# Performance work log

Measured on AMD Instinct MI355X. Metric: run time of the kernel, lower is better.

Reference implementation:

```python
import jax, jax.numpy as jnp
import numpy as np

N, T, F_IN, H, D_FF, C_OUT = 4096, 60, 64, 128, 256, 1


def _gru_layer(x_tnf, W_ih, W_hh, b_ih, b_hh):
    # torch nn.GRU single layer; x_tnf: [T, N, in]
    def step(h, xt):
        gi = xt @ W_ih.T + b_ih          # [N, 3H]
        gh = h @ W_hh.T + b_hh
        i_r, i_z, i_n = jnp.split(gi, 3, axis=-1)
        h_r, h_z, h_n = jnp.split(gh, 3, axis=-1)
        r = jax.nn.sigmoid(i_r + h_r)
        z = jax.nn.sigmoid(i_z + h_z)
        n = jnp.tanh(i_n + r * h_n)
        h = (1.0 - z) * n + z * h
        return h, h
    h0 = jnp.zeros((x_tnf.shape[1], W_hh.shape[1]), x_tnf.dtype)
    hT, ys = jax.lax.scan(step, h0, x_tnf)
    return hT, ys


def setup_inputs() -> dict:
    key = jax.random.key(0)
    ks = jax.random.split(key, 20)
    s_in = 1.0 / np.sqrt(F_IN)
    s_h = 1.0 / np.sqrt(H)
    inp = {
        'x': jax.random.normal(ks[0], (N, T, F_IN), jnp.float32),
        'W_ih0': jax.random.normal(ks[1], (3 * H, F_IN), jnp.float32) * s_in,
        'W_hh0': jax.random.normal(ks[2], (3 * H, H), jnp.float32) * s_h,
        'b_ih0': jax.random.normal(ks[3], (3 * H,), jnp.float32) * s_h,
        'b_hh0': jax.random.normal(ks[4], (3 * H,), jnp.float32) * s_h,
        'W_ih1': jax.random.normal(ks[5], (3 * H, H), jnp.float32) * s_h,
        'W_hh1': jax.random.normal(ks[6], (3 * H, H), jnp.float32) * s_h,
        'b_ih1': jax.random.normal(ks[7], (3 * H,), jnp.float32) * s_h,
        'b_hh1': jax.random.normal(ks[8], (3 * H,), jnp.float32) * s_h,
        'Wt': jax.random.normal(ks[9], (H, H), jnp.float32) * s_h,
        'bt': jax.random.normal(ks[10], (H,), jnp.float32) * s_h,
        'a': jax.random.normal(ks[11], (2 * H, 1), jnp.float32),
        'Wfc': jax.random.normal(ks[12], (H, H), jnp.float32) * s_h,
        'bfc': jax.random.normal(ks[13], (H,), jnp.float32) * s_h,
        'Wp1': jax.random.normal(ks[14], (D_FF, H), jnp.float32) * s_h,
        'bp1': jax.random.normal(ks[15], (D_FF,), jnp.float32) * s_h,
        'Wp2': jax.random.normal(ks[16], (C_OUT, D_FF), jnp.float32) * (1.0 / np.sqrt(D_FF)),
        'bp2': jax.random.normal(ks[17], (C_OUT,), jnp.float32) * (1.0 / np.sqrt(D_FF)),
    }
    return inp


def reference(x, W_ih0, W_hh0, b_ih0, b_hh0, W_ih1, W_hh1, b_ih1, b_hh1,
              Wt, bt, a, Wfc, bfc, Wp1, bp1, Wp2, bp2):
    x_tnf = jnp.transpose(x, (1, 0, 2))  # [T, N, F]
    _, ys0 = _gru_layer(x_tnf, W_ih0, W_hh0, b_ih0, b_hh0)
    hT, _ = _gru_layer(ys0, W_ih1, W_hh1, b_ih1, b_hh1)
    hidden = hT  # out[:, -1, :], [N, H]

    # cal_attention: score[i,j] = a[:H].x_j + a[H:].x_i  (separable GAT score)
    xt = hidden @ Wt.T + bt                      # transformation(x) == transformation(y)
    a_flat = a[:, 0]
    s_j = xt @ a_flat[:H]                        # [N], contributes per-column
    s_i = xt @ a_flat[H:]                        # [N], contributes per-row
    scores = jax.nn.leaky_relu(s_i[:, None] + s_j[None, :], negative_slope=0.01)
    att = jax.nn.softmax(scores, axis=1)         # [N, N]

    hidden = att @ hidden + hidden
    hidden = jax.nn.leaky_relu(hidden @ Wfc.T + bfc, negative_slope=0.01)
    h1 = jax.nn.gelu(hidden @ Wp1.T + bp1, approximate=False)
    out = h1 @ Wp2.T + bp2                       # [N, 1]
    return jnp.squeeze(out)                      # [N]
```

## Files before the change

kernel.cpp:

```cpp
#include <hip/hip_runtime.h>
#include <cstdint>
#include <cstddef>

#define TSTEPS 60
#define NB 4096
#define HD 128

typedef __attribute__((ext_vector_type(8))) short short8;
typedef __attribute__((ext_vector_type(4))) float f32x4;

#define WS_SJ    0
#define WS_SI    16384
#define WS_HID   32768
#define WS_HTH   2129920
#define WS_HTL   3178496
#define WS_F0H   4227072
#define WS_F0L   (WS_F0H+49152)
#define WS_FR0H  (WS_F0L+49152)
#define WS_FR0L  (WS_FR0H+98304)
#define WS_FR1H  (WS_FR0L+98304)
#define WS_FR1L  (WS_FR1H+98304)
#define WS_FR2H  (WS_FR1L+98304)
#define WS_FR2L  (WS_FR2H+98304)
#define WS_BASE  (WS_FR2L+98304)
#define WS_Y0P   WS_BASE
#define WS_FULL  (WS_Y0P + 125829120ULL)

__device__ __forceinline__ float b2f(unsigned short h){ return __uint_as_float(((unsigned)h)<<16); }
__device__ __forceinline__ unsigned short f2b(float f){
  unsigned u = __float_as_uint(f);
  u = (u + 0x7FFFu + ((u>>16)&1u)) >> 16;
  return (unsigned short)u;
}
__device__ __forceinline__ float sigm(float x){ return 1.0f/(1.0f + __expf(-x)); }
__device__ __forceinline__ float tanhfast(float x){
  float xc = fminf(fmaxf(x,-15.0f),15.0f);
  float e = __expf(2.0f*xc);
  return (e-1.0f)/(e+1.0f);
}
__device__ __forceinline__ float lrelu(float x){ return x > 0.0f ? x : 0.01f*x; }
__device__ __forceinline__ float ldr1(const void* p, size_t i, int f32){
  return f32 ? ((const float*)p)[i] : b2f(((const unsigned short*)p)[i]);
}
template<bool F32>
__device__ __forceinline__ float4 ldg4c(const void* p, size_t i){
  if (F32) return *(const float4*)((const float*)p + i);
  ushort4 u = *(const ushort4*)((const unsigned short*)p + i);
  float4 f; f.x=b2f(u.x); f.y=b2f(u.y); f.z=b2f(u.z); f.w=b2f(u.w); return f;
}
__device__ __forceinline__ f32x4 f4zero(){ f32x4 v = {0.f,0.f,0.f,0.f}; return v; }
__device__ __forceinline__ void pinv(short8& v){ asm volatile("" : "+v"(v)); }

__device__ __forceinline__ void ldsbar(){
  asm volatile("s_waitcnt lgkmcnt(0)\n\ts_barrier" ::: "memory");
}

__device__ int probe_f32(const void* p, int nprobe, volatile int* s){
  if (threadIdx.x == 0) *s = 0;
  __syncthreads();
  if ((int)threadIdx.x < nprobe) {
    float v = b2f(((const unsigned short*)p)[threadIdx.x]);
    if (!(v == v) || fabsf(v) > 1e4f) *s = 1;
  }
  __syncthreads();
  int r = *s;
  __syncthreads();
  return r;
}

__global__ void diag_kernel(float* out, float code){
  int i = blockIdx.x*256 + threadIdx.x;
  if (i < 4096) out[i] = code;
}

__device__ void repack_mat(const void* src, int f32, int K, int nks,
                           unsigned short* hi, unsigned short* lo,
                           int tid, int nthr){
  int total = 384*K;
  for (int idx = tid; idx < total; idx += nthr) {
    int j = idx & 7, lane = (idx>>3)&63, t = idx>>9;
    int ks = t % nks, g = (t/nks)%3, w = t/(nks*3);
    int row = 16*(w + 8*g) + (lane & 15);
    int k   = ks*32 + ((lane>>4)<<3) + j;
    float v = f32 ? ((const float*)src)[(size_t)row*K + k]
                  : b2f(((const unsigned short*)src)[(size_t)row*K + k]);
    unsigned short h = f2b(v);
    hi[idx] = h;
    lo[idx] = f2b(v - b2f(h));
  }
}

__global__ __launch_bounds__(256) void repack_kernel(
    const void* wih0, const void* whh0, const void* wih1, const void* whh1,
    char* ws)
{
  __shared__ int sp;
  int f0 = probe_f32(wih0, 256, &sp);
  int f1 = probe_f32(whh0, 256, &sp);
  int f2 = probe_f32(wih1, 256, &sp);
  int f3 = probe_f32(whh1, 256, &sp);
  int tid  = blockIdx.x*256 + threadIdx.x;
  int nthr = gridDim.x*256;
  repack_mat(wih0, f0,  64, 2, (unsigned short*)(ws+WS_F0H),  (unsigned short*)(ws+WS_F0L),  tid, nthr);
  repack_mat(whh0, f1, 128, 4, (unsigned short*)(ws+WS_FR0H), (unsigned short*)(ws+WS_FR0L), tid, nthr);
  repack_mat(wih1, f2, 128, 4, (unsigned short*)(ws+WS_FR1H), (unsigned short*)(ws+WS_FR1L), tid, nthr);
  repack_mat(whh1, f3, 128, 4, (unsigned short*)(ws+WS_FR2H), (unsigned short*)(ws+WS_FR2L), tid, nthr);
}

#define MFMA __builtin_amdgcn_mfma_f32_16x16x32_bf16

__global__ __launch_bounds__(512) __attribute__((amdgpu_waves_per_eu(2,2)))
void gru0_kernel(const void* __restrict__ xg,
                 const void* __restrict__ bih0, const void* __restrict__ bhh0,
                 const char* __restrict__ ws, unsigned* __restrict__ y0p)
{
  __shared__ __align__(16) unsigned short xbh[2][1152], xbl[2][1152];
  __shared__ __align__(16) unsigned short hbh[2][2176], hbl[2][2176];
  __shared__ int sp;
  const int tid  = threadIdx.x;
  const int w    = tid >> 6;
  const int lane = tid & 63;
  const int ln   = lane & 15;
  const int kq   = lane >> 4;
  const int r0   = blockIdx.x * 16;

  int xf  = probe_f32(xg,   256, &sp);
  int fb0 = probe_f32(bih0, 256, &sp);
  int fh0 = probe_f32(bhh0, 256, &sp);

  const unsigned short* f0h  = (const unsigned short*)(ws+WS_F0H);
  const unsigned short* f0l  = (const unsigned short*)(ws+WS_F0L);
  const unsigned short* fr0h = (const unsigned short*)(ws+WS_FR0H);
  const unsigned short* fr0l = (const unsigned short*)(ws+WS_FR0L);

  short8 X0h[3][2], X0l[3][2];
  #pragma unroll
  for (int g = 0; g < 3; ++g)
    #pragma unroll
    for (int ks = 0; ks < 2; ++ks) {
      int fi = (w*3+g)*2 + ks;
      X0h[g][ks] = *(const short8*)&f0h[fi*512 + lane*8];
      X0l[g][ks] = *(const short8*)&f0l[fi*512 + lane*8];
      pinv(X0h[g][ks]); pinv(X0l[g][ks]);
    }

  short8 R0h[3][4], R0l[3][4];
  #pragma unroll
  for (int g = 0; g < 3; ++g)
    #pragma unroll
    for (int ks = 0; ks < 4; ++ks) {
      int fi = (w*3+g)*4 + ks;
      R0h[g][ks] = *(const short8*)&fr0h[fi*512 + lane*8];
      R0l[g][ks] = *(const short8*)&fr0l[fi*512 + lane*8];
      pinv(R0h[g][ks]); pinv(R0l[g][ks]);
    }

  const int nr = 16*w + ln;
  float brc0 = ldr1(bih0,nr,fb0)     + ldr1(bhh0,nr,fh0);
  float bzc0 = ldr1(bih0,nr+128,fb0) + ldr1(bhh0,nr+128,fh0);
  float bin0 = ldr1(bih0,nr+256,fb0);
  float bhn0 = ldr1(bhh0,nr+256,fh0);

  for (int i = tid; i < 2176; i += 512) { hbh[0][i] = 0; hbl[0][i] = 0; }
  const int xm = tid >> 5, xfc = (tid & 31)*2;
  #pragma unroll
  for (int tt = 0; tt < 2; ++tt) {
    size_t base = ((size_t)(r0+xm)*TSTEPS + tt)*64 + xfc;
    float v0, v1;
    if (xf) { float2 xv = *(const float2*)((const float*)xg + base); v0 = xv.x; v1 = xv.y; }
    else { ushort2 u = *(const ushort2*)((const unsigned short*)xg + base); v0 = b2f(u.x); v1 = b2f(u.y); }
    unsigned short a0 = f2b(v0), a1 = f2b(v1);
    unsigned short l0 = f2b(v0-b2f(a0)), l1 = f2b(v1-b2f(a1));
    *(unsigned*)&xbh[tt][xm*72+xfc] = (unsigned)a0 | ((unsigned)a1<<16);
    *(unsigned*)&xbl[tt][xm*72+xfc] = (unsigned)l0 | ((unsigned)l1<<16);
  }
  float h0o[4] = {0.f,0.f,0.f,0.f};
  __syncthreads();

  f32x4 accX[3];
  #pragma unroll
  for (int g = 0; g < 3; ++g) accX[g] = f4zero();
  #pragma unroll
  for (int ks = 0; ks < 2; ++ks) {
    short8 axh = *(const short8*)&xbh[0][ln*72 + ks*32 + kq*8];
    short8 axl = *(const short8*)&xbl[0][ln*72 + ks*32 + kq*8];
    #pragma unroll
    for (int g = 0; g < 3; ++g) {
      accX[g] = MFMA(axh, X0h[g][ks], accX[g], 0,0,0);
      accX[g] = MFMA(axh, X0l[g][ks], accX[g], 0,0,0);
      accX[g] = MFMA(axl, X0h[g][ks], accX[g], 0,0,0);
    }
  }

  #pragma unroll 1
  for (int t = 0; t < TSTEPS; ++t) {
    const int b0 = t & 1, b1 = b0 ^ 1;
    unsigned short pa0=0, pa1=0, pl0=0, pl1=0;
    if (t+2 < TSTEPS) {
      size_t base = ((size_t)(r0+xm)*TSTEPS + (t+2))*64 + xfc;
      float v0, v1;
      if (xf) { float2 xv = *(const float2*)((const float*)xg + base); v0 = xv.x; v1 = xv.y; }
      else { ushort2 u = *(const ushort2*)((const unsigned short*)xg + base); v0 = b2f(u.x); v1 = b2f(u.y); }
      pa0 = f2b(v0); pa1 = f2b(v1);
      pl0 = f2b(v0-b2f(pa0)); pl1 = f2b(v1-b2f(pa1));
    }

    f32x4 acc[4];
    acc[0] = accX[0]; acc[1] = accX[1]; acc[2] = accX[2]; acc[3] = f4zero();
    #pragma unroll
    for (int ks = 0; ks < 4; ++ks) {
      short8 ahh = *(const short8*)&hbh[b0][ln*136 + ks*32 + kq*8];
      short8 ahl = *(const short8*)&hbl[b0][ln*136 + ks*32 + kq*8];
      #pragma unroll
      for (int g = 0; g < 3; ++g) {
        int tgt = (g==2) ? 3 : g;
        acc[tgt] = MFMA(ahh, R0h[g][ks], acc[tgt], 0,0,0);
        acc[tgt] = MFMA(ahh, R0l[g][ks], acc[tgt], 0,0,0);
        acc[tgt] = MFMA(ahl, R0h[g][ks], acc[tgt], 0,0,0);
      }
    }
    unsigned short nh[4], nl[4];
    #pragma unroll
    for (int rg = 0; rg < 4; ++rg) {
      float r  = sigm(acc[0][rg] + brc0);
      float z  = sigm(acc[1][rg] + bzc0);
      float nn = tanhfast(acc[2][rg] + bin0 + r*(acc[3][rg] + bhn0));
      float h  = nn + z*(h0o[rg] - nn);
      h0o[rg] = h;
      unsigned short hh = f2b(h);
      nh[rg] = hh; nl[rg] = f2b(h - b2f(hh));
    }
    {
      size_t ybase = ((size_t)blockIdx.x*TSTEPS + t)*2048;
      #pragma unroll
      for (int rg = 0; rg < 4; ++rg)
        y0p[ybase + (kq*4+rg)*128 + w*16 + ln] =
            (unsigned)nh[rg] | ((unsigned)nl[rg] << 16);
    }
    #pragma unroll
    for (int rg = 0; rg < 4; ++rg) {
      int off = (kq*4+rg)*136 + w*16 + ln;
      hbh[b1][off] = nh[rg]; hbl[b1][off] = nl[rg];
    }
    if (t+2 < TSTEPS) {
      *(unsigned*)&xbh[b0][xm*72+xfc] = (unsigned)pa0 | ((unsigned)pa1<<16);
      *(unsigned*)&xbl[b0][xm*72+xfc] = (unsigned)pl0 | ((unsigned)pl1<<16);
    }
    if (t+1 < TSTEPS) {
      #pragma unroll
      for (int g = 0; g < 3; ++g) accX[g] = f4zero();
      #pragma unroll
      for (int ks = 0; ks < 2; ++ks) {
        short8 axh = *(const short8*)&xbh[b1][ln*72 + ks*32 + kq*8];
        short8 axl = *(const short8*)&xbl[b1][ln*72 + ks*32 + kq*8];
        #pragma unroll
        for (int g = 0; g < 3; ++g) {
          accX[g] = MFMA(axh, X0h[g][ks], accX[g], 0,0,0);
          accX[g] = MFMA(axh, X0l[g][ks], accX[g], 0,0,0);
          accX[g] = MFMA(axl, X0h[g][ks], accX[g], 0,0,0);
        }
      }
    }
    ldsbar();
  }
}

__global__ __launch_bounds__(512) __attribute__((amdgpu_waves_per_eu(2,2)))
void gru1_kernel(const void* __restrict__ bih1, const void* __restrict__ bhh1,
                 const char* __restrict__ ws, const unsigned* __restrict__ y0p,
                 float* __restrict__ hidg,
                 unsigned short* __restrict__ hTh, unsigned short* __restrict__ hTl)
{
  __shared__ __align__(16) unsigned short wih1hL[49152];
  __shared__ __align__(16) unsigned short ybh[2][2176], ybl[2][2176];
  __shared__ __align__(16) unsigned short h1bh[2][2176], h1bl[2][2176];
  __shared__ int sp;
  const int tid  = threadIdx.x;
  const int w    = tid >> 6;
  const int lane = tid & 63;
  const int ln   = lane & 15;
  const int kq   = lane >> 4;
  const int r0   = blockIdx.x * 16;

  int fb1 = probe_f32(bih1, 256, &sp);
  int fh1 = probe_f32(bhh1, 256, &sp);

  const unsigned short* fr1h = (const unsigned short*)(ws+WS_FR1H);
  const unsigned short* fr1l = (const unsigned short*)(ws+WS_FR1L);
  const unsigned short* fr2h = (const unsigned short*)(ws+WS_FR2H);
  const unsigned short* fr2l = (const unsigned short*)(ws+WS_FR2L);

  for (int i = tid*8; i < 49152; i += 4096) {
    *(ushort4*)&wih1hL[i]   = *(const ushort4*)&fr1h[i];
    *(ushort4*)&wih1hL[i+4] = *(const ushort4*)&fr1h[i+4];
  }

  short8 W1hp[2][4];
  #pragma unroll
  for (int g = 0; g < 2; ++g)
    #pragma unroll
    for (int ks = 0; ks < 4; ++ks) {
      W1hp[g][ks] = *(const short8*)&fr1h[((w*3+g)*4+ks)*512 + lane*8];
      pinv(W1hp[g][ks]);
    }

  short8 W1l[3][4], R2h[3][4], R2l[3][4];
  #pragma unroll
  for (int g = 0; g < 3; ++g)
    #pragma unroll
    for (int ks = 0; ks < 4; ++ks) {
      int fi = (w*3+g)*4 + ks;
      W1l[g][ks] = *(const short8*)&fr1l[fi*512 + lane*8];
      R2h[g][ks] = *(const short8*)&fr2h[fi*512 + lane*8];
      R2l[g][ks] = *(const short8*)&fr2l[fi*512 + lane*8];
      pinv(W1l[g][ks]); pinv(R2h[g][ks]); pinv(R2l[g][ks]);
    }

  const int nr = 16*w + ln;
  float brc1 = ldr1(bih1,nr,fb1)     + ldr1(bhh1,nr,fh1);
  float bzc1 = ldr1(bih1,nr+128,fb1) + ldr1(bhh1,nr+128,fh1);
  float bin1 = ldr1(bih1,nr+256,fb1);
  float bhn1 = ldr1(bhh1,nr+256,fh1);

  for (int i = tid; i < 2176; i += 512) { h1bh[0][i] = 0; h1bl[0][i] = 0; }
  const int yi4 = tid*4, yrow = yi4 >> 7, ycol = yi4 & 127;
  {
    uint4 pv = *(const uint4*)&y0p[((size_t)blockIdx.x*TSTEPS + 0)*2048 + yi4];
    ushort4 vh, vl;
    vh.x=(unsigned short)(pv.x&0xffff); vl.x=(unsigned short)(pv.x>>16);
    vh.y=(unsigned short)(pv.y&0xffff); vl.y=(unsigned short)(pv.y>>16);
    vh.z=(unsigned short)(pv.z&0xffff); vl.z=(unsigned short)(pv.z>>16);
    vh.w=(unsigned short)(pv.w&0xffff); vl.w=(unsigned short)(pv.w>>16);
    *(ushort4*)&ybh[0][yrow*136+ycol] = vh;
    *(ushort4*)&ybl[0][yrow*136+ycol] = vl;
  }
  float h1o[4] = {0.f,0.f,0.f,0.f};
  __syncthreads();

  #pragma unroll 1
  for (int t = 0; t < TSTEPS; ++t) {
    const int b0 = t & 1, b1 = b0 ^ 1;
    uint4 pv = {0,0,0,0};
    if (t+1 < TSTEPS)
      pv = *(const uint4*)&y0p[((size_t)blockIdx.x*TSTEPS + (t+1))*2048 + yi4];

    f32x4 acc[4];
    #pragma unroll
    for (int g = 0; g < 4; ++g) acc[g] = f4zero();
    #pragma unroll
    for (int ks = 0; ks < 4; ++ks) {
      short8 ayh = *(const short8*)&ybh[b0][ln*136 + ks*32 + kq*8];
      short8 ayl = *(const short8*)&ybl[b0][ln*136 + ks*32 + kq*8];
      short8 a1h = *(const short8*)&h1bh[b0][ln*136 + ks*32 + kq*8];
      short8 a1l = *(const short8*)&h1bl[b0][ln*136 + ks*32 + kq*8];
      #pragma unroll
      for (int g = 0; g < 3; ++g) {
        int tgtI = (g==2) ? 2 : g;
        int tgtH = (g==2) ? 3 : g;
        short8 bh;
        if (g < 2) bh = W1hp[g][ks];
        else       bh = *(const short8*)&wih1hL[((w*3+2)*4+ks)*512 + lane*8];
        acc[tgtI] = MFMA(ayh, bh,         acc[tgtI], 0,0,0);
        acc[tgtI] = MFMA(ayh, W1l[g][ks], acc[tgtI], 0,0,0);
        acc[tgtI] = MFMA(ayl, bh,         acc[tgtI], 0,0,0);
        acc[tgtH] = MFMA(a1h, R2h[g][ks], acc[tgtH], 0,0,0);
        acc[tgtH] = MFMA(a1h, R2l[g][ks], acc[tgtH], 0,0,0);
        acc[tgtH] = MFMA(a1l, R2h[g][ks], acc[tgtH], 0,0,0);
      }
    }
    unsigned short nh[4], nl[4];
    #pragma unroll
    for (int rg = 0; rg < 4; ++rg) {
      float r  = sigm(acc[0][rg] + brc1);
      float z  = sigm(acc[1][rg] + bzc1);
      float nn = tanhfast(acc[2][rg] + bin1 + r*(acc[3][rg] + bhn1));
      float h  = nn + z*(h1o[rg] - nn);
      h1o[rg] = h;
      unsigned short hh = f2b(h);
      nh[rg] = hh; nl[rg] = f2b(h - b2f(hh));
    }
    #pragma unroll
    for (int rg = 0; rg < 4; ++rg) {
      int off = (kq*4+rg)*136 + w*16 + ln;
      h1bh[b1][off] = nh[rg]; h1bl[b1][off] = nl[rg];
    }
    if (t+1 < TSTEPS) {
      ushort4 vh, vl;
      vh.x=(unsigned short)(pv.x&0xffff); vl.x=(unsigned short)(pv.x>>16);
      vh.y=(unsigned short)(pv.y&0xffff); vl.y=(unsigned short)(pv.y>>16);
      vh.z=(unsigned short)(pv.z&0xffff); vl.z=(unsigned short)(pv.z>>16);
      vh.w=(unsigned short)(pv.w&0xffff); vl.w=(unsigned short)(pv.w>>16);
      *(ushort4*)&ybh[b1][yrow*136+ycol] = vh;
      *(ushort4*)&ybl[b1][yrow*136+ycol] = vl;
    }
    ldsbar();
  }

  {
    int c = w*16 + ln;
    #pragma unroll
    for (int rg = 0; rg < 4; ++rg)
      hidg[(size_t)(r0 + kq*4 + rg)*HD + c] = h1o[rg];
    ushort4 ph, pl;
    unsigned short* hh = (unsigned short*)&ph;
    unsigned short* ll = (unsigned short*)&pl;
    #pragma unroll
    for (int rg = 0; rg < 4; ++rg) {
      hh[rg] = f2b(h1o[rg]);
      ll[rg] = f2b(h1o[rg] - b2f(hh[rg]));
    }
    size_t o = (size_t)c*NB + r0 + kq*4;
    *(ushort4*)&hTh[o] = ph;
    *(ushort4*)&hTl[o] = pl;
  }
}

__global__ __launch_bounds__(512, 1) void gru_fb_kernel(
    const void* __restrict__ xg,
    const void* __restrict__ bih0, const void* __restrict__ bhh0,
    const void* __restrict__ bih1, const void* __restrict__ bhh1,
    const char* __restrict__ ws, float* __restrict__ hidg,
    unsigned short* __restrict__ hTh, unsigned short* __restrict__ hTl)
{
  __shared__ __align__(16) unsigned short wih0L[49152];
  __shared__ __align__(16) unsigned short xhi[1152], xlo[1152];
  __shared__ __align__(16) unsigned short h0hi[2176], h0lo[2176];
  __shared__ __align__(16) unsigned short h1hi[2176], h1lo[2176];
  __shared__ int sp;
  const int tid  = threadIdx.x;
  const int w    = tid >> 6;
  const int lane = tid & 63;
  const int ln   = lane & 15;
  const int kq   = lane >> 4;
  const int r0   = blockIdx.x * 16;

  int xf  = probe_f32(xg,   256, &sp);
  int fb0 = probe_f32(bih0, 256, &sp);
  int fh0 = probe_f32(bhh0, 256, &sp);
  int fb1 = probe_f32(bih1, 256, &sp);
  int fh1 = probe_f32(bhh1, 256, &sp);

  const unsigned short* f0h  = (const unsigned short*)(ws+WS_F0H);
  const unsigned short* f0l  = (const unsigned short*)(ws+WS_F0L);
  const unsigned short* fr0h = (const unsigned short*)(ws+WS_FR0H);
  const unsigned short* fr0l = (const unsigned short*)(ws+WS_FR0L);
  const unsigned short* fr1h = (const unsigned short*)(ws+WS_FR1H);
  const unsigned short* fr1l = (const unsigned short*)(ws+WS_FR1L);
  const unsigned short* fr2h = (const unsigned short*)(ws+WS_FR2H);
  const unsigned short* fr2l = (const unsigned short*)(ws+WS_FR2L);

  for (int i = tid*8; i < 24576; i += 4096) {
    *(ushort4*)&wih0L[i]         = *(const ushort4*)&f0h[i];
    *(ushort4*)&wih0L[i+4]       = *(const ushort4*)&f0h[i+4];
    *(ushort4*)&wih0L[24576+i]   = *(const ushort4*)&f0l[i];
    *(ushort4*)&wih0L[24576+i+4] = *(const ushort4*)&f0l[i+4];
  }
  short8 R0h[3][4], R1h[3][4], R2h[3][4];
  #pragma unroll
  for (int g = 0; g < 3; ++g)
    #pragma unroll
    for (int ks = 0; ks < 4; ++ks) {
      int fi = (w*3+g)*4 + ks;
      R0h[g][ks] = *(const short8*)&fr0h[fi*512 + lane*8];
      R1h[g][ks] = *(const short8*)&fr1h[fi*512 + lane*8];
      R2h[g][ks] = *(const short8*)&fr2h[fi*512 + lane*8];
      pinv(R0h[g][ks]); pinv(R1h[g][ks]); pinv(R2h[g][ks]);
    }
  const int nr = 16*w + ln;
  float brc0 = ldr1(bih0,nr,fb0)     + ldr1(bhh0,nr,fh0);
  float bzc0 = ldr1(bih0,nr+128,fb0) + ldr1(bhh0,nr+128,fh0);
  float bin0 = ldr1(bih0,nr+256,fb0);
  float bhn0 = ldr1(bhh0,nr+256,fh0);
  float brc1 = ldr1(bih1,nr,fb1)     + ldr1(bhh1,nr,fh1);
  float bzc1 = ldr1(bih1,nr+128,fb1) + ldr1(bhh1,nr+128,fh1);
  float bin1 = ldr1(bih1,nr+256,fb1);
  float bhn1 = ldr1(bhh1,nr+256,fh1);

  for (int i = tid; i < 2176; i += 512) {
    h0hi[i] = 0; h0lo[i] = 0; h1hi[i] = 0; h1lo[i] = 0;
  }
  float h0o[4] = {0.f,0.f,0.f,0.f};
  float h1o[4] = {0.f,0.f,0.f,0.f};
  __syncthreads();

  #pragma unroll 1
  for (int t = 0; t < TSTEPS; ++t) {
    {
      int i0 = tid*2, m = i0 >> 6, f = i0 & 63;
      size_t base = ((size_t)(r0+m)*TSTEPS + t)*64 + f;
      float v0, v1;
      if (xf) { float2 xv = *(const float2*)((const float*)xg + base); v0 = xv.x; v1 = xv.y; }
      else { ushort2 u = *(const ushort2*)((const unsigned short*)xg + base); v0 = b2f(u.x); v1 = b2f(u.y); }
      unsigned short a0 = f2b(v0), a1 = f2b(v1);
      xhi[m*72+f] = a0;              xhi[m*72+f+1] = a1;
      xlo[m*72+f] = f2b(v0-b2f(a0)); xlo[m*72+f+1] = f2b(v1-b2f(a1));
    }
    __syncthreads();
    f32x4 acc[4];
    #pragma unroll
    for (int g = 0; g < 4; ++g) acc[g] = f4zero();
    #pragma unroll
    for (int ks = 0; ks < 2; ++ks) {
      short8 axh = *(const short8*)&xhi[ln*72 + ks*32 + kq*8];
      short8 axl = *(const short8*)&xlo[ln*72 + ks*32 + kq*8];
      #pragma unroll
      for (int g = 0; g < 3; ++g) {
        int fi = (w*3+g)*2 + ks;
        short8 bh = *(const short8*)&wih0L[fi*512 + lane*8];
        short8 bl = *(const short8*)&wih0L[24576 + fi*512 + lane*8];
        acc[g] = MFMA(axh, bh, acc[g], 0,0,0);
        acc[g] = MFMA(axh, bl, acc[g], 0,0,0);
        acc[g] = MFMA(axl, bh, acc[g], 0,0,0);
      }
    }
    #pragma unroll
    for (int ks = 0; ks < 4; ++ks) {
      short8 ahh = *(const short8*)&h0hi[ln*136 + ks*32 + kq*8];
      short8 ahl = *(const short8*)&h0lo[ln*136 + ks*32 + kq*8];
      #pragma unroll
      for (int g = 0; g < 3; ++g) {
        int tgt = (g==2) ? 3 : g;
        short8 bl = *(const short8*)&fr0l[((w*3+g)*4+ks)*512 + lane*8];
        acc[tgt] = MFMA(ahh, R0h[g][ks], acc[tgt], 0,0,0);
        acc[tgt] = MFMA(ahh, bl,         acc[tgt], 0,0,0);
        acc[tgt] = MFMA(ahl, R0h[g][ks], acc[tgt], 0,0,0);
      }
    }
    unsigned short nh[4], nl[4];
    #pragma unroll
    for (int rg = 0; rg < 4; ++rg) {
      float r  = sigm(acc[0][rg] + brc0);
      float z  = sigm(acc[1][rg] + bzc0);
      float nn = tanhfast(acc[2][rg] + bin0 + r*(acc[3][rg] + bhn0));
      float h  = nn + z*(h0o[rg] - nn);
      h0o[rg] = h;
      unsigned short hh = f2b(h);
      nh[rg] = hh; nl[rg] = f2b(h - b2f(hh));
    }
    __syncthreads();
    #pragma unroll
    for (int rg = 0; rg < 4; ++rg) {
      int off = (kq*4+rg)*136 + w*16 + ln;
      h0hi[off] = nh[rg]; h0lo[off] = nl[rg];
    }
    __syncthreads();
    #pragma unroll
    for (int g = 0; g < 4; ++g) acc[g] = f4zero();
    #pragma unroll
    for (int ks = 0; ks < 4; ++ks) {
      short8 ayh = *(const short8*)&h0hi[ln*136 + ks*32 + kq*8];
      short8 ayl = *(const short8*)&h0lo[ln*136 + ks*32 + kq*8];
      short8 a1h = *(const short8*)&h1hi[ln*136 + ks*32 + kq*8];
      short8 a1l = *(const short8*)&h1lo[ln*136 + ks*32 + kq*8];
      #pragma unroll
      for (int g = 0; g < 3; ++g) {
        int tgtI = (g==2) ? 2 : g;
        int tgtH = (g==2) ? 3 : g;
        short8 blI = *(const short8*)&fr1l[((w*3+g)*4+ks)*512 + lane*8];
        short8 blH = *(const short8*)&fr2l[((w*3+g)*4+ks)*512 + lane*8];
        acc[tgtI] = MFMA(ayh, R1h[g][ks], acc[tgtI], 0,0,0);
        acc[tgtI] = MFMA(ayh, blI,        acc[tgtI], 0,0,0);
        acc[tgtI] = MFMA(ayl, R1h[g][ks], acc[tgtI], 0,0,0);
        acc[tgtH] = MFMA(a1h, R2h[g][ks], acc[tgtH], 0,0,0);
        acc[tgtH] = MFMA(a1h, blH,        acc[tgtH], 0,0,0);
        acc[tgtH] = MFMA(a1l, R2h[g][ks], acc[tgtH], 0,0,0);
      }
    }
    #pragma unroll
    for (int rg = 0; rg < 4; ++rg) {
      float r  = sigm(acc[0][rg] + brc1);
      float z  = sigm(acc[1][rg] + bzc1);
      float nn = tanhfast(acc[2][rg] + bin1 + r*(acc[3][rg] + bhn1));
      float h  = nn + z*(h1o[rg] - nn);
      h1o[rg] = h;
      unsigned short hh = f2b(h);
      nh[rg] = hh; nl[rg] = f2b(h - b2f(hh));
    }
    __syncthreads();
    #pragma unroll
    for (int rg = 0; rg < 4; ++rg) {
      int off = (kq*4+rg)*136 + w*16 + ln;
      h1hi[off] = nh[rg]; h1lo[off] = nl[rg];
    }
  }
  {
    int c = w*16 + ln;
    #pragma unroll
    for (int rg = 0; rg < 4; ++rg)
      hidg[(size_t)(r0 + kq*4 + rg)*HD + c] = h1o[rg];
    ushort4 ph, pl;
    unsigned short* hh = (unsigned short*)&ph;
    unsigned short* ll = (unsigned short*)&pl;
    #pragma unroll
    for (int rg = 0; rg < 4; ++rg) {
      hh[rg] = f2b(h1o[rg]);
      ll[rg] = f2b(h1o[rg] - b2f(hh[rg]));
    }
    size_t o = (size_t)c*NB + r0 + kq*4;
    *(ushort4*)&hTh[o] = ph;
    *(ushort4*)&hTl[o] = pl;
  }
}

template<bool WT32>
__device__ void sprep_body(
    const float* hidg, const void* wt, const void* bt, const void* a,
    int f_bt, int f_a, float* sjg, float* sig, float* hL, float* redb)
{
  const int tid = threadIdx.x;
  const int r0  = blockIdx.x * 16;
  for (int i = tid; i < 2048; i += 256) hL[i] = hidg[(size_t)r0*128 + i];
  __syncthreads();
  const int r = tid >> 4, cg = tid & 15, c0 = cg*8;
  float sjp = 0.f, sip = 0.f;
  #pragma unroll 1
  for (int cc = 0; cc < 8; ++cc) {
    int cI = c0 + cc;
    float acc = ldr1(bt, cI, f_bt);
    #pragma unroll 4
    for (int kq = 0; kq < 32; ++kq) {
      int k = kq*4;
      float4 wv = ldg4c<WT32>(wt, (size_t)cI*128 + k);
      float4 h = *(const float4*)&hL[r*128 + k];
      acc += wv.x*h.x + wv.y*h.y + wv.z*h.z + wv.w*h.w;
    }
    sjp += acc * ldr1(a, cI, f_a);
    sip += acc * ldr1(a, cI + 128, f_a);
  }
  redb[(r*16+cg)*2]   = sjp;
  redb[(r*16+cg)*2+1] = sip;
  __syncthreads();
  if (tid < 32) {
    int r2 = tid >> 1, wh = tid & 1;
    float s = 0.f;
    for (int g = 0; g < 16; ++g) s += redb[(r2*16+g)*2 + wh];
    if (wh == 0) sjg[r0+r2] = s; else sig[r0+r2] = s;
  }
}

__global__ __launch_bounds__(256) void sprep_kernel(
    const float* hidg, const void* wt, const void* bt, const void* a,
    float* sjg, float* sig)
{
  __shared__ float hL[2048];
  __shared__ float redb[512];
  __shared__ int sp;
  int f_wt = probe_f32(wt, 256, &sp);
  int f_bt = probe_f32(bt, 128, &sp);
  int f_a  = probe_f32(a,  256, &sp);
  if (f_wt) sprep_body<true >(hidg, wt, bt, a, f_bt, f_a, sjg, sig, hL, redb);
  else      sprep_body<false>(hidg, wt, bt, a, f_bt, f_a, sjg, sig, hL, redb);
}

template<bool PW32>
__device__ void attn_body(
    const float* sjg, const float* sig, const float* hidg,
    const unsigned short* hTh, const unsigned short* hTl,
    const void* wfc, const void* bfc, const void* wp1, const void* bp1,
    const void* wp2, const void* bp2,
    int f_bfc, int f_bp1, int f_wp2, float* outg,
    float* sjs, unsigned short* Pbuf, float* Obuf, float* redm,
    float* siL, float* miL, float* Zb)
{
  const int tid = threadIdx.x;
  const int w = tid >> 6, lane = tid & 63, ln = lane & 15, kq = lane >> 4;
  const int r0 = blockIdx.x * 16;

  for (int i = tid; i < 4096; i += 512) sjs[i] = sjg[i];
  __syncthreads();
  float mx = -1e30f;
  for (int i = tid; i < 4096; i += 512) mx = fmaxf(mx, sjs[i]);
  redm[tid] = mx;
  __syncthreads();
  for (int s = 256; s > 0; s >>= 1) {
    if (tid < s) redm[tid] = fmaxf(redm[tid], redm[tid+s]);
    __syncthreads();
  }
  if (tid < 16) {
    float si = sig[r0 + tid];
    siL[tid] = si;
    miL[tid] = lrelu(si + redm[0]);
  }
  __syncthreads();

  float zp[16];
  #pragma unroll
  for (int i = 0; i < 16; ++i) zp[i] = 0.f;
  f32x4 accO = f4zero();
  const int col = w*16 + ln;

  #define GENP(CH, BASE)                                                    \
    {                                                                       \
      unsigned short* Phi_ = (BASE);                                        \
      unsigned short* Plo_ = (BASE) + 8320;                                 \
      float sjv = sjs[(CH)*512 + tid];                                      \
      _Pragma("unroll")                                                     \
      for (int i = 0; i < 16; ++i) {                                        \
        float v = lrelu(siL[i] + sjv);                                      \
        float p = __expf(v - miL[i]);                                       \
        zp[i] += p;                                                         \
        unsigned short hh = f2b(p);                                         \
        Phi_[i*520 + tid] = hh;                                             \
        Plo_[i*520 + tid] = f2b(p - b2f(hh));                               \
      }                                                                     \
    }

  GENP(0, Pbuf);
  __syncthreads();

  #pragma unroll 1
  for (int ch = 0; ch < 8; ++ch) {
    const int b = ch & 1;
    unsigned short* Phi = Pbuf + b*16640;
    unsigned short* Plo = Phi + 8320;
    #pragma unroll
    for (int ks = 0; ks < 16; ++ks) {
      short8 Ah = *(const short8*)&Phi[ln*520 + ks*32 + kq*8];
      short8 Al = *(const short8*)&Plo[ln*520 + ks*32 + kq*8];
      size_t bo = (size_t)col*NB + ch*512 + ks*32 + kq*8;
      short8 Bh = *(const short8*)&hTh[bo];
      short8 Bl = *(const short8*)&hTl[bo];
      accO = MFMA(Ah, Bh, accO, 0,0,0);
      accO = MFMA(Ah, Bl, accO, 0,0,0);
      accO = MFMA(Al, Bh, accO, 0,0,0);
    }
    if (ch < 7) GENP(ch+1, Pbuf + (b^1)*16640);
    __syncthreads();
  }
  #undef GENP

  #pragma unroll
  for (int rg = 0; rg < 4; ++rg)
    Obuf[(kq*4+rg)*128 + col] = accO[rg];

  float* zarr = (float*)Pbuf;
  #pragma unroll
  for (int i = 0; i < 16; ++i) zarr[i*512 + tid] = zp[i];
  __syncthreads();
  {
    int row = tid >> 5, t0 = tid & 31;
    float s = 0.f;
    #pragma unroll
    for (int k = 0; k < 16; ++k) s += zarr[row*512 + t0 + 32*k];
    redm[row*32 + t0] = s;
  }
  __syncthreads();
  if (tid < 16) {
    float s = 0.f;
    for (int g = 0; g < 32; ++g) s += redm[tid*32 + g];
    Zb[tid] = s;
  }
  __syncthreads();

  {
    int e0 = tid*4, row = e0 >> 7, c = e0 & 127;
    float zi = Zb[row];
    #pragma unroll
    for (int e = 0; e < 4; ++e)
      Obuf[e0+e] = Obuf[e0+e]/zi + hidg[(size_t)(r0+row)*128 + c + e];
  }
  __syncthreads();

  float* h3f = sjs;
  {
    int o0 = tid*4, row = o0 >> 7, c = o0 & 127;
    #pragma unroll 1
    for (int e = 0; e < 4; ++e) {
      int cI = c + e;
      float acc = ldr1(bfc, cI, f_bfc);
      #pragma unroll 4
      for (int k4 = 0; k4 < 32; ++k4) {
        int k = k4*4;
        float4 wv = ldg4c<PW32>(wfc, (size_t)cI*128 + k);
        float4 h = *(const float4*)&Obuf[row*128 + k];
        acc += wv.x*h.x + wv.y*h.y + wv.z*h.z + wv.w*h.w;
      }
      h3f[row*128 + cI] = lrelu(acc);
    }
  }
  __syncthreads();

  float* h1f = (float*)Pbuf;
  {
    int o0 = tid*8, row = o0 >> 8, c = o0 & 255;
    #pragma unroll 1
    for (int e = 0; e < 8; ++e) {
      int cI = c + e;
      float acc = ldr1(bp1, cI, f_bp1);
      #pragma unroll 4
      for (int k4 = 0; k4 < 32; ++k4) {
        int k = k4*4;
        float4 wv = ldg4c<PW32>(wp1, (size_t)cI*128 + k);
        float4 h = *(const float4*)&h3f[row*128 + k];
        acc += wv.x*h.x + wv.y*h.y + wv.z*h.z + wv.w*h.w;
      }
      h1f[row*256 + cI] = 0.5f*acc*(1.0f + erff(acc*0.70710678118f));
    }
  }
  __syncthreads();

  {
    int row = tid >> 5, t0 = tid & 31;
    float s = 0.f;
    #pragma unroll
    for (int k = 0; k < 8; ++k) {
      int cI = t0 + 32*k;
      s += h1f[row*256 + cI] * ldr1(wp2, cI, f_wp2);
    }
    redm[row*32 + t0] = s;
  }
  __syncthreads();
  if (tid < 16) {
    float acc = ldr1(bp2, 0, f_bp1);
    for (int g = 0; g < 32; ++g) acc += redm[tid*32 + g];
    outg[r0 + tid] = acc;
  }
}

__global__ __launch_bounds__(512) void attn_kernel(
    const float* sjg, const float* sig, const float* hidg,
    const unsigned short* hTh, const unsigned short* hTl,
    const void* wfc, const void* bfc, const void* wp1, const void* bp1,
    const void* wp2, const void* bp2, float* outg)
{
  __shared__ float sjs[4096];
  __shared__ __align__(16) unsigned short Pbuf[33280];
  __shared__ float Obuf[2048];
  __shared__ float redm[512];
  __shared__ float siL[16], miL[16], Zb[16];
  __shared__ int sp;
  int f_wfc = probe_f32(wfc, 256, &sp);
  int f_bfc = probe_f32(bfc, 128, &sp);
  int f_bp1 = probe_f32(bp1, 256, &sp);
  int f_wp2 = probe_f32(wp2, 256, &sp);
  if (f_wfc) attn_body<true >(sjg, sig, hidg, hTh, hTl, wfc, bfc, wp1, bp1,
                              wp2, bp2, f_bfc, f_bp1, f_wp2, outg,
                              sjs, Pbuf, Obuf, redm, siL, miL, Zb);
  else       attn_body<false>(sjg, sig, hidg, hTh, hTl, wfc, bfc, wp1, bp1,
                              wp2, bp2, f_bfc, f_bp1, f_wp2, outg,
                              sjs, Pbuf, Obuf, redm, siL, miL, Zb);
}

extern "C" void kernel_launch(void* const* d_in, const int* in_sizes, int n_in,
                              void* d_out, int out_size, void* d_ws, size_t ws_size,
                              hipStream_t stream)
{
  float* out = (float*)d_out;
  const int expected[18] = {15728640,24576,49152,384,384,49152,49152,384,384,
                            16384,128,256,16384,128,32768,256,256,1};
  int bad = 0;
  if (n_in != 18 || out_size != 4096) bad = 1600;
  else for (int i = 0; i < 18; ++i) if (in_sizes[i] != expected[i]) { bad = 1600; break; }
  if (!bad && ws_size < (size_t)WS_BASE) bad = 1664;
  if (bad) { diag_kernel<<<16, 256, 0, stream>>>(out, (float)bad); return; }

  char* ws = (char*)d_ws;
  float*          sj  = (float*)(ws + WS_SJ);
  float*          si  = (float*)(ws + WS_SI);
  float*          hid = (float*)(ws + WS_HID);
  unsigned short* hTh = (unsigned short*)(ws + WS_HTH);
  unsigned short* hTl = (unsigned short*)(ws + WS_HTL);

  repack_kernel<<<256, 256, 0, stream>>>(d_in[1], d_in[2], d_in[5], d_in[6], ws);
  if (ws_size >= WS_FULL) {
    unsigned* y0p = (unsigned*)(ws + WS_Y0P);
    gru0_kernel<<<256, 512, 0, stream>>>(d_in[0], d_in[3], d_in[4], ws, y0p);
    gru1_kernel<<<256, 512, 0, stream>>>(d_in[7], d_in[8], ws, y0p,
                                         hid, hTh, hTl);
  } else {
    gru_fb_kernel<<<256, 512, 0, stream>>>(d_in[0], d_in[3], d_in[4],
                                           d_in[7], d_in[8], ws, hid, hTh, hTl);
  }
  sprep_kernel<<<256, 256, 0, stream>>>(hid, d_in[9], d_in[10], d_in[11], sj, si);
  attn_kernel<<<256, 512, 0, stream>>>(sj, si, hid, hTh, hTl,
                                       d_in[12], d_in[13], d_in[14], d_in[15],
                                       d_in[16], d_in[17], out);
}
```

Baseline: 590.5 us.

## Split GRU layer-0 K dimension across wave pairs with LDS partial-sum exchange

Doubles gru0 block size to 1024 threads so each pair of waves splits the reduction dimension of the input and recurrent matmuls in half. The partial accumulators are exchanged through a new shared-memory buffer, and each wave then finishes the gate math for two of the four rows. It also drops the one-step-ahead input projection and stages x only one step ahead. The aim is to shorten the serial per-timestep MFMA chain, at the cost of an extra barrier and LDS round-trip every step, and fewer registers per thread.

```diff
diff --git a/kernel.cpp b/kernel.cpp
--- a/kernel.cpp
+++ b/kernel.cpp
@@ -109,16 +109,19 @@
 
 #define MFMA __builtin_amdgcn_mfma_f32_16x16x32_bf16
 
-__global__ __launch_bounds__(512) __attribute__((amdgpu_waves_per_eu(2,2)))
+__global__ __launch_bounds__(1024)
 void gru0_kernel(const void* __restrict__ xg,
                  const void* __restrict__ bih0, const void* __restrict__ bhh0,
                  const char* __restrict__ ws, unsigned* __restrict__ y0p)
 {
   __shared__ __align__(16) unsigned short xbh[2][1152], xbl[2][1152];
   __shared__ __align__(16) unsigned short hbh[2][2176], hbl[2][2176];
+  __shared__ __align__(16) float pex[8192];
   __shared__ int sp;
   const int tid  = threadIdx.x;
-  const int w    = tid >> 6;
+  const int W    = tid >> 6;
+  const int cg   = W >> 1;
+  const int kh   = W & 1;
   const int lane = tid & 63;
   const int ln   = lane & 15;
   const int kq   = lane >> 4;
@@ -133,133 +136,150 @@
   const unsigned short* fr0h = (const unsigned short*)(ws+WS_FR0H);
   const unsigned short* fr0l = (const unsigned short*)(ws+WS_FR0L);
 
-  short8 X0h[3][2], X0l[3][2];
+  short8 X0h[3], X0l[3];
+  #pragma unroll
+  for (int g = 0; g < 3; ++g) {
+    int fi = (cg*3+g)*2 + kh;
+    X0h[g] = *(const short8*)&f0h[fi*512 + lane*8];
+    X0l[g] = *(const short8*)&f0l[fi*512 + lane*8];
+    pinv(X0h[g]); pinv(X0l[g]);
+  }
+  short8 R0h[3][2], R0l[3][2];
   #pragma unroll
   for (int g = 0; g < 3; ++g)
     #pragma unroll
-    for (int ks = 0; ks < 2; ++ks) {
-      int fi = (w*3+g)*2 + ks;
-      X0h[g][ks] = *(const short8*)&f0h[fi*512 + lane*8];
-      X0l[g][ks] = *(const short8*)&f0l[fi*512 + lane*8];
-      pinv(X0h[g][ks]); pinv(X0l[g][ks]);
-    }
-
-  short8 R0h[3][4], R0l[3][4];
-  #pragma unroll
-  for (int g = 0; g < 3; ++g)
-    #pragma unroll
-    for (int ks = 0; ks < 4; ++ks) {
-      int fi = (w*3+g)*4 + ks;
-      R0h[g][ks] = *(const short8*)&fr0h[fi*512 + lane*8];
-      R0l[g][ks] = *(const short8*)&fr0l[fi*512 + lane*8];
-      pinv(R0h[g][ks]); pinv(R0l[g][ks]);
-    }
-
-  const int nr = 16*w + ln;
+    for (int jj = 0; jj < 2; ++jj) {
+      int fi = (cg*3+g)*4 + kh*2 + jj;
+      R0h[g][jj] = *(const short8*)&fr0h[fi*512 + lane*8];
+      R0l[g][jj] = *(const short8*)&fr0l[fi*512 + lane*8];
+      pinv(R0h[g][jj]); pinv(R0l[g][jj]);
+    }
+
+  const int nr = cg*16 + ln;
   float brc0 = ldr1(bih0,nr,fb0)     + ldr1(bhh0,nr,fh0);
   float bzc0 = ldr1(bih0,nr+128,fb0) + ldr1(bhh0,nr+128,fh0);
   float bin0 = ldr1(bih0,nr+256,fb0);
   float bhn0 = ldr1(bhh0,nr+256,fh0);
 
-  for (int i = tid; i < 2176; i += 512) { hbh[0][i] = 0; hbl[0][i] = 0; }
+  for (int i = tid; i < 2176; i += 1024) { hbh[0][i] = 0; hbl[0][i] = 0; }
   const int xm = tid >> 5, xfc = (tid & 31)*2;
-  #pragma unroll
-  for (int tt = 0; tt < 2; ++tt) {
-    size_t base = ((size_t)(r0+xm)*TSTEPS + tt)*64 + xfc;
+  if (tid < 512) {
+    size_t base = ((size_t)(r0+xm)*TSTEPS + 0)*64 + xfc;
     float v0, v1;
     if (xf) { float2 xv = *(const float2*)((const float*)xg + base); v0 = xv.x; v1 = xv.y; }
     else { ushort2 u = *(const ushort2*)((const unsigned short*)xg + base); v0 = b2f(u.x); v1 = b2f(u.y); }
     unsigned short a0 = f2b(v0), a1 = f2b(v1);
     unsigned short l0 = f2b(v0-b2f(a0)), l1 = f2b(v1-b2f(a1));
-    *(unsigned*)&xbh[tt][xm*72+xfc] = (unsigned)a0 | ((unsigned)a1<<16);
-    *(unsigned*)&xbl[tt][xm*72+xfc] = (unsigned)l0 | ((unsigned)l1<<16);
-  }
-  float h0o[4] = {0.f,0.f,0.f,0.f};
-  __syncthreads();
-
-  f32x4 accX[3];
-  #pragma unroll
-  for (int g = 0; g < 3; ++g) accX[g] = f4zero();
-  #pragma unroll
-  for (int ks = 0; ks < 2; ++ks) {
-    short8 axh = *(const short8*)&xbh[0][ln*72 + ks*32 + kq*8];
-    short8 axl = *(const short8*)&xbl[0][ln*72 + ks*32 + kq*8];
-    #pragma unroll
-    for (int g = 0; g < 3; ++g) {
-      accX[g] = MFMA(axh, X0h[g][ks], accX[g], 0,0,0);
-      accX[g] = MFMA(axh, X0l[g][ks], accX[g], 0,0,0);
-      accX[g] = MFMA(axl, X0h[g][ks], accX[g], 0,0,0);
-    }
-  }
+    *(unsigned*)&xbh[0][xm*72+xfc] = (unsigned)a0 | ((unsigned)a1<<16);
+    *(unsigned*)&xbl[0][xm*72+xfc] = (unsigned)l0 | ((unsigned)l1<<16);
+  }
+  float h0o[2] = {0.f, 0.f};
+  __syncthreads();
 
   #pragma unroll 1
   for (int t = 0; t < TSTEPS; ++t) {
     const int b0 = t & 1, b1 = b0 ^ 1;
-    unsigned short pa0=0, pa1=0, pl0=0, pl1=0;
-    if (t+2 < TSTEPS) {
-      size_t base = ((size_t)(r0+xm)*TSTEPS + (t+2))*64 + xfc;
-      float v0, v1;
+    float v0 = 0.f, v1 = 0.f;
+    const bool stg = (tid < 512) && (t+1 < TSTEPS);
+    if (stg) {
+      size_t base = ((size_t)(r0+xm)*TSTEPS + (t+1))*64 + xfc;
       if (xf) { float2 xv = *(const float2*)((const float*)xg + base); v0 = xv.x; v1 = xv.y; }
       else { ushort2 u = *(const ushort2*)((const unsigned short*)xg + base); v0 = b2f(u.x); v1 = b2f(u.y); }
-      pa0 = f2b(v0); pa1 = f2b(v1);
-      pl0 = f2b(v0-b2f(pa0)); pl1 = f2b(v1-b2f(pa1));
     }
 
     f32x4 acc[4];
-    acc[0] = accX[0]; acc[1] = accX[1]; acc[2] = accX[2]; acc[3] = f4zero();
-    #pragma unroll
-    for (int ks = 0; ks < 4; ++ks) {
-      short8 ahh = *(const short8*)&hbh[b0][ln*136 + ks*32 + kq*8];
-      short8 ahl = *(const short8*)&hbl[b0][ln*136 + ks*32 + kq*8];
+    #pragma unroll
+    for (int g = 0; g < 4; ++g) acc[g] = f4zero();
+    {
+      short8 axh = *(const short8*)&xbh[b0][ln*72 + kh*32 + kq*8];
+      short8 axl = *(const short8*)&xbl[b0][ln*72 + kh*32 + kq*8];
+      #pragma unroll
+      for (int g = 0; g < 3; ++g) {
+        acc[g] = MFMA(axh, X0h[g], acc[g], 0,0,0);
+        acc[g] = MFMA(axh, X0l[g], acc[g], 0,0,0);
+        acc[g] = MFMA(axl, X0h[g], acc[g], 0,0,0);
+      }
+    }
+    #pragma unroll
+    for (int jj = 0; jj < 2; ++jj) {
+      short8 ahh = *(const short8*)&hbh[b0][ln*136 + (kh*2+jj)*32 + kq*8];
+      short8 ahl = *(const short8*)&hbl[b0][ln*136 + (kh*2+jj)*32 + kq*8];
       #pragma unroll
       for (int g = 0; g < 3; ++g) {
         int tgt = (g==2) ? 3 : g;
-        acc[tgt] = MFMA(ahh, R0h[g][ks], acc[tgt], 0,0,0);
-        acc[tgt] = MFMA(ahh, R0l[g][ks], acc[tgt], 0,0,0);
-        acc[tgt] = MFMA(ahl, R0h[g][ks], acc[tgt], 0,0,0);
-      }
-    }
-    unsigned short nh[4], nl[4];
-    #pragma unroll
-    for (int rg = 0; rg < 4; ++rg) {
-      float r  = sigm(acc[0][rg] + brc0);
-      float z  = sigm(acc[1][rg] + bzc0);
-      float nn = tanhfast(acc[2][rg] + bin0 + r*(acc[3][rg] + bhn0));
-      float h  = nn + z*(h0o[rg] - nn);
-      h0o[rg] = h;
+        acc[tgt] = MFMA(ahh, R0h[g][jj], acc[tgt], 0,0,0);
+        acc[tgt] = MFMA(ahh, R0l[g][jj], acc[tgt], 0,0,0);
+        acc[tgt] = MFMA(ahl, R0h[g][jj], acc[tgt], 0,0,0);
+      }
+    }
+
+    {
+      int wbase = W*512 + lane*2;
+      if (kh == 0) {
+        #pragma unroll
+        for (int g = 0; g < 4; ++g) {
+          float2 wv; wv.x = acc[g][2]; wv.y = acc[g][3];
+          *(float2*)&pex[wbase + g*128] = wv;
+        }
+      } else {
+        #pragma unroll
+        for (int g = 0; g < 4; ++g) {
+          float2 wv; wv.x = acc[g][0]; wv.y = acc[g][1];
+          *(float2*)&pex[wbase + g*128] = wv;
+        }
+      }
+    }
+    ldsbar();
+
+    float c0[2], c1[2], c2[2], c3[2];
+    {
+      int pbase = (W^1)*512 + lane*2;
+      float2 p0 = *(const float2*)&pex[pbase];
+      float2 p1 = *(const float2*)&pex[pbase + 128];
+      float2 p2 = *(const float2*)&pex[pbase + 256];
+      float2 p3 = *(const float2*)&pex[pbase + 384];
+      if (kh == 0) {
+        c0[0]=acc[0][0]+p0.x; c0[1]=acc[0][1]+p0.y;
+        c1[0]=acc[1][0]+p1.x; c1[1]=acc[1][1]+p1.y;
+        c2[0]=acc[2][0]+p2.x; c2[1]=acc[2][1]+p2.y;
+        c3[0]=acc[3][0]+p3.x; c3[1]=acc[3][1]+p3.y;
+      } else {
+        c0[0]=acc[0][2]+p0.x; c0[1]=acc[0][3]+p0.y;
+        c1[0]=acc[1][2]+p1.x; c1[1]=acc[1][3]+p1.y;
+        c2[0]=acc[2][2]+p2.x; c2[1]=acc[2][3]+p2.y;
+        c3[0]=acc[3][2]+p3.x; c3[1]=acc[3][3]+p3.y;
+      }
+    }
+
+    unsigned short nh2[2], nl2[2];
+    #pragma unroll
+    for (int j = 0; j < 2; ++j) {
+      float r  = sigm(c0[j] + brc0);
+      float z  = sigm(c1[j] + bzc0);
+      float nn = tanhfast(c2[j] + bin0 + r*(c3[j] + bhn0));
+      float h  = nn + z*(h0o[j] - nn);
+      h0o[j] = h;
       unsigned short hh = f2b(h);
-      nh[rg] = hh; nl[rg] = f2b(h - b2f(hh));
-    }
+      nh2[j] = hh; nl2[j] = f2b(h - b2f(hh));
+    }
+    const int rowb = kq*4 + kh*2;
     {
       size_t ybase = ((size_t)blockIdx.x*TSTEPS + t)*2048;
       #pragma unroll
-      for (int rg = 0; rg < 4; ++rg)
-        y0p[ybase + (kq*4+rg)*128 + w*16 + ln] =
-            (unsigned)nh[rg] | ((unsigned)nl[rg] << 16);
-    }
-    #pragma unroll
-    for (int rg = 0; rg < 4; ++rg) {
-      int off = (kq*4+rg)*136 + w*16 + ln;
-      hbh[b1][off] = nh[rg]; hbl[b1][off] = nl[rg];
-    }
-    if (t+2 < TSTEPS) {
-      *(unsigned*)&xbh[b0][xm*72+xfc] = (unsigned)pa0 | ((unsigned)pa1<<16);
-      *(unsigned*)&xbl[b0][xm*72+xfc] = (unsigned)pl0 | ((unsigned)pl1<<16);
-    }
-    if (t+1 < TSTEPS) {
-      #pragma unroll
-      for (int g = 0; g < 3; ++g) accX[g] = f4zero();
-      #pragma unroll
-      for (int ks = 0; ks < 2; ++ks) {
-        short8 axh = *(const short8*)&xbh[b1][ln*72 + ks*32 + kq*8];
-        short8 axl = *(const short8*)&xbl[b1][ln*72 + ks*32 + kq*8];
-        #pragma unroll
-        for (int g = 0; g < 3; ++g) {
-          accX[g] = MFMA(axh, X0h[g][ks], accX[g], 0,0,0);
-          accX[g] = MFMA(axh, X0l[g][ks], accX[g], 0,0,0);
-          accX[g] = MFMA(axl, X0h[g][ks], accX[g], 0,0,0);
-        }
-      }
+      for (int j = 0; j < 2; ++j)
+        y0p[ybase + (rowb+j)*128 + cg*16 + ln] =
+            (unsigned)nh2[j] | ((unsigned)nl2[j] << 16);
+    }
+    #pragma unroll
+    for (int j = 0; j < 2; ++j) {
+      int off = (rowb+j)*136 + cg*16 + ln;
+      hbh[b1][off] = nh2[j]; hbl[b1][off] = nl2[j];
+    }
+    if (stg) {
+      unsigned short a0 = f2b(v0), a1 = f2b(v1);
+      unsigned short l0 = f2b(v0-b2f(a0)), l1 = f2b(v1-b2f(a1));
+      *(unsigned*)&xbh[b1][xm*72+xfc] = (unsigned)a0 | ((unsigned)a1<<16);
+      *(unsigned*)&xbl[b1][xm*72+xfc] = (unsigned)l0 | ((unsigned)l1<<16);
     }
     ldsbar();
   }
@@ -864,7 +884,7 @@
   repack_kernel<<<256, 256, 0, stream>>>(d_in[1], d_in[2], d_in[5], d_in[6], ws);
   if (ws_size >= WS_FULL) {
     unsigned* y0p = (unsigned*)(ws + WS_Y0P);
-    gru0_kernel<<<256, 512, 0, stream>>>(d_in[0], d_in[3], d_in[4], ws, y0p);
+    gru0_kernel<<<256, 1024, 0, stream>>>(d_in[0], d_in[3], d_in[4], ws, y0p);
     gru1_kernel<<<256, 512, 0, stream>>>(d_in[7], d_in[8], ws, y0p,
                                          hid, hTh, hTl);
   } else {
```

Result: faster. 566.0 us (-4.2%).
